# Kernel optimization log

Hardware: AMD Instinct MI355X
Metric: run time of the kernel (lower is better)

Reference implementation:

```python
import jax, jax.numpy as jnp
import numpy as np


def log_g(x):
    # log of g(x) where g(x) = x + 0.5 for x >= 0 else sigmoid(x)
    return jnp.where(x >= 0, jnp.log(jnp.where(x >= 0, x, 0.0) + 0.5), -jax.nn.softplus(-x))


def mingru_layer(x, h0, W, b):
    # x: (B,S,Din), h0: (B,1,H) positive, W: (2H,Din), b: (2H,)
    gh = jnp.einsum('bsd,ed->bse', x, W) + b
    gate, hidden = jnp.split(gh, 2, axis=-1)
    log_z = -jax.nn.softplus(-gate)        # log sigmoid(gate)
    log_coeffs = -jax.nn.softplus(gate)    # log (1 - sigmoid(gate))
    log_values = jnp.concatenate([jnp.log(h0), log_z + log_g(hidden)], axis=1)  # (B,S+1,H)
    a_star = jnp.pad(jnp.cumsum(log_coeffs, axis=1), ((0, 0), (1, 0), (0, 0)))  # (B,S+1,H)
    log_h = a_star + jax.lax.cumlogsumexp(log_values - a_star, axis=1)
    return jnp.exp(log_h)[:, 1:]  # (B,S,H)


def setup_inputs() -> dict:
    key = jax.random.key(0)
    ks = jax.random.split(key, 6)
    B, S, D, H = 8, 2048, 1024, 1024
    L = 2
    s = 0.02
    return {
        'x': jax.random.normal(ks[0], (B, S, D), jnp.float32),
        'h': jax.random.uniform(ks[1], (L, B, 1, H), jnp.float32, 0.05, 1.0),
        'w0': jax.random.normal(ks[2], (2 * H, D), jnp.float32) * s,
        'b0': jax.random.normal(ks[3], (2 * H,), jnp.float32) * s,
        'w1': jax.random.normal(ks[4], (2 * H, H), jnp.float32) * s,
        'b1': jax.random.normal(ks[5], (2 * H,), jnp.float32) * s,
    }


def reference(x, h, w0, b0, w1, b1):
    # layer 0 (residual, align = Identity since input_dims == hidden_dims)
    out0 = mingru_layer(x, h[0], w0, b0)
    h0_final = out0[:, -1:]
    inp = out0 + x
    # layer 1 (last layer: residual, no dropout after)
    out1 = mingru_layer(inp, h[1], w1, b1)
    h1_final = out1[:, -1:]
    out = out1 + inp
    h_final = jnp.stack([h0_final, h1_final])  # (L,B,1,H)
    return out, h_final
```

## Files before the change

kernel.cpp:

```cpp
#include <hip/hip_runtime.h>
#include <hip/hip_bf16.h>
#include <cstdint>
#include <cstddef>

#define GAS __attribute__((address_space(1)))
#define LAS __attribute__((address_space(3)))

typedef __attribute__((ext_vector_type(8))) __bf16 bf16x8;
typedef __attribute__((ext_vector_type(4))) float f32x4;

constexpr int kB = 8, kS = 2048, kK = 1024, kH = 1024;
constexpr int kM = kB * kS;
constexpr int kN2 = 2 * kH;
constexpr int kChunks = 64;
constexpr int kSc = kS / kChunks;

constexpr int BM = 256, BN = 256, BK = 32;
constexpr int NKT = kK / BK;

constexpr size_t kOffXb   = 0;
constexpr size_t kOffW0   = 33554432;
constexpr size_t kOffW1   = 37748736;
constexpr size_t kOffA    = 41943040;
constexpr size_t kOffG    = 75497472;
constexpr size_t kOffCA   = 109051904;
constexpr size_t kOffCV   = 111149056;
constexpr size_t kOffHst  = 113246208;
constexpr size_t kWsNeed  = 115343360;

__device__ __forceinline__ ushort f2bf(float f) {
    union { float f; uint32_t u; } v; v.f = f;
    uint32_t r = v.u + 0x7FFFu + ((v.u >> 16) & 1u);
    return (ushort)(r >> 16);
}
__device__ __forceinline__ float bf2f(ushort u) {
    union { uint32_t u; float f; } v; v.u = (uint32_t)u << 16;
    return v.f;
}

__global__ void cvt_bf16_kernel(const float* __restrict__ src, ushort* __restrict__ dst, int n4) {
    int i = blockIdx.x * blockDim.x + threadIdx.x;
    if (i >= n4) return;
    f32x4 v = *reinterpret_cast<const f32x4*>(src + (size_t)i * 4);
    ushort4 o;
    o.x = f2bf(v.x); o.y = f2bf(v.y); o.z = f2bf(v.z); o.w = f2bf(v.w);
    *reinterpret_cast<ushort4*>(dst + (size_t)i * 4) = o;
}

__global__ __launch_bounds__(512, 1)
void gemm_epi_kernel(const ushort* __restrict__ A, const ushort* __restrict__ W,
                     const float* __restrict__ bias,
                     ushort* __restrict__ abuf, ushort* __restrict__ gbuf)
{
    __shared__ ushort smem[65536];

    const int tid  = threadIdx.x;
    const int lane = tid & 63;
    const int wv   = tid >> 6;
    const int wm   = wv >> 2;
    const int wn   = wv & 3;

    const int bid = blockIdx.x;
    const int sid = (bid & 7) * 64 + (bid >> 3);
    const int tm  = sid >> 3;
    const int tn  = sid & 7;
    const int m0  = tm * BM;
    const int n0  = tn * BN;

    f32x4 acc[8][4];
#pragma unroll
    for (int i = 0; i < 8; ++i)
#pragma unroll
        for (int j = 0; j < 4; ++j) acc[i][j] = (f32x4){0.f, 0.f, 0.f, 0.f};

    const int srow  = wv * 16 + (lane >> 2);
    const int sslot = (lane & 3) ^ ((lane >> 3) & 3);
    const int scol  = sslot * 8;

    const ushort* ga0 = A + (size_t)(m0 + srow) * kK + scol;
    const ushort* ga1 = ga0 + (size_t)128 * kK;
    const ushort* gb0 = W + (size_t)(n0 + srow) * kK + scol;
    const ushort* gb1 = gb0 + (size_t)128 * kK;

    char* lds = (char*)smem;
    const int ldsw = wv * 1024;

    const int rslot = (lane >> 4) ^ ((lane >> 1) & 3);
    const int rb    = (lane & 15) * 64 + rslot * 16;
    const int aoff  = wm * 8192 + rb;
    const int boff  = 16384 + wn * 4096 + rb;

#define VMWAIT(N) asm volatile("s_waitcnt vmcnt(" #N ")" ::: "memory")

#define STAGE_A(SBUF) do {                                                       \
    __builtin_amdgcn_global_load_lds((const GAS void*)(ga0),                     \
        (LAS void*)(lds + (SBUF) * 32768 + ldsw),          16, 0, 0);            \
    __builtin_amdgcn_global_load_lds((const GAS void*)(ga1),                     \
        (LAS void*)(lds + (SBUF) * 32768 + 8192  + ldsw),  16, 0, 0);            \
  } while (0)

#define STAGE_B(SBUF) do {                                                       \
    __builtin_amdgcn_global_load_lds((const GAS void*)(gb0),                     \
        (LAS void*)(lds + (SBUF) * 32768 + 16384 + ldsw),  16, 0, 0);            \
    __builtin_amdgcn_global_load_lds((const GAS void*)(gb1),                     \
        (LAS void*)(lds + (SBUF) * 32768 + 24576 + ldsw),  16, 0, 0);            \
    ga0 += BK; ga1 += BK; gb0 += BK; gb1 += BK;                                  \
  } while (0)

#define TILE_GEN(BUF, SA, SB, EW) do {                                           \
    bf16x8 bf_[4], af_[4];                                                       \
    _Pragma("unroll")                                                            \
    for (int nf_ = 0; nf_ < 4; ++nf_)                                            \
        bf_[nf_] = *reinterpret_cast<const bf16x8*>(                             \
            lds + (BUF) * 32768 + boff + nf_ * 1024);                            \
    _Pragma("unroll")                                                            \
    for (int mf_ = 0; mf_ < 4; ++mf_)                                            \
        af_[mf_] = *reinterpret_cast<const bf16x8*>(                             \
            lds + (BUF) * 32768 + aoff + mf_ * 1024);                            \
    SA;                                                                          \
    __builtin_amdgcn_s_barrier();                                                \
    asm volatile("s_waitcnt lgkmcnt(0)" ::: "memory");                           \
    __builtin_amdgcn_sched_barrier(0);                                           \
    __builtin_amdgcn_s_setprio(1);                                               \
    _Pragma("unroll")                                                            \
    for (int mf_ = 0; mf_ < 4; ++mf_)                                            \
        _Pragma("unroll")                                                        \
        for (int nf_ = 0; nf_ < 4; ++nf_)                                        \
            acc[mf_][nf_] = __builtin_amdgcn_mfma_f32_16x16x32_bf16(             \
                af_[mf_], bf_[nf_], acc[mf_][nf_], 0, 0, 0);                     \
    __builtin_amdgcn_s_setprio(0);                                               \
    __builtin_amdgcn_s_barrier();                                                \
    _Pragma("unroll")                                                            \
    for (int mf_ = 0; mf_ < 4; ++mf_)                                            \
        af_[mf_] = *reinterpret_cast<const bf16x8*>(                             \
            lds + (BUF) * 32768 + aoff + 4096 + mf_ * 1024);                     \
    SB;                                                                          \
    __builtin_amdgcn_s_barrier();                                                \
    asm volatile("s_waitcnt lgkmcnt(0)" ::: "memory");                           \
    __builtin_amdgcn_sched_barrier(0);                                           \
    __builtin_amdgcn_s_setprio(1);                                               \
    _Pragma("unroll")                                                            \
    for (int mf_ = 0; mf_ < 4; ++mf_)                                            \
        _Pragma("unroll")                                                        \
        for (int nf_ = 0; nf_ < 4; ++nf_)                                        \
            acc[4 + mf_][nf_] = __builtin_amdgcn_mfma_f32_16x16x32_bf16(         \
                af_[mf_], bf_[nf_], acc[4 + mf_][nf_], 0, 0, 0);                 \
    __builtin_amdgcn_s_setprio(0);                                               \
    EW;                                                                          \
    __builtin_amdgcn_s_barrier();                                                \
  } while (0)

#define TILE(BUF, SBUF) TILE_GEN(BUF, STAGE_A(SBUF), STAGE_B(SBUF), VMWAIT(4))
#define TAIL0(BUF)      TILE_GEN(BUF, (void)0, (void)0, VMWAIT(0))
#define TAIL1(BUF)      TILE_GEN(BUF, (void)0, (void)0, (void)0)

    STAGE_A(0); STAGE_B(0);
    STAGE_A(1); STAGE_B(1);
    VMWAIT(4);
    __builtin_amdgcn_s_barrier();

    for (int g = 0; g < 7; ++g) {
        TILE(0, 2);
        TILE(1, 3);
        TILE(2, 0);
        TILE(3, 1);
    }
    TILE(0, 2);
    TILE(1, 3);
    TAIL0(2);
    TAIL1(3);

#undef TILE
#undef TAIL0
#undef TAIL1
#undef TILE_GEN
#undef STAGE_A
#undef STAGE_B
#undef VMWAIT

    const bool isGate = (tn < 4);
    ushort* outp = isGate ? abuf : gbuf;
    const int ncol0 = (isGate ? tn : tn - 4) * 256 + wn * 64;
    float bn[4];
#pragma unroll
    for (int nf = 0; nf < 4; ++nf) bn[nf] = bias[n0 + wn * 64 + nf * 16 + (lane & 15)];
#pragma unroll
    for (int mf = 0; mf < 8; ++mf) {
#pragma unroll
        for (int i = 0; i < 4; ++i) {
            const int m = m0 + wm * 128 + mf * 16 + (lane >> 4) * 4 + i;
            ushort* rowp = outp + (size_t)m * kH + ncol0;
#pragma unroll
            for (int nf = 0; nf < 4; ++nf) {
                float val = acc[mf][nf][i] + bn[nf];
                float r;
                if (isGate) r = 1.f / (1.f + __expf(val));
                else        r = (val >= 0.f) ? val + 0.5f : 1.f / (1.f + __expf(-val));
                rowp[nf * 16 + (lane & 15)] = f2bf(r);
            }
        }
    }
}

__global__ void scan_reduce_kernel(const ushort* __restrict__ abuf, const ushort* __restrict__ gbuf,
                                   float* __restrict__ cA, float* __restrict__ cV)
{
    int idx = blockIdx.x * 256 + threadIdx.x;
    int chg = idx & 255;
    int c   = (idx >> 8) & (kChunks - 1);
    int b   = idx >> 14;
    size_t ch = (size_t)chg * 4;
    size_t row = (size_t)b * kS + (size_t)c * kSc;
    const ushort* ap = abuf + row * kH + ch;
    const ushort* gp = gbuf + row * kH + ch;
    f32x4 A = (f32x4){1.f, 1.f, 1.f, 1.f};
    f32x4 V = (f32x4){0.f, 0.f, 0.f, 0.f};
    for (int t = 0; t < kSc; ++t) {
        ushort4 au = *reinterpret_cast<const ushort4*>(ap);
        ushort4 gu = *reinterpret_cast<const ushort4*>(gp);
        f32x4 a = (f32x4){bf2f(au.x), bf2f(au.y), bf2f(au.z), bf2f(au.w)};
        f32x4 g = (f32x4){bf2f(gu.x), bf2f(gu.y), bf2f(gu.z), bf2f(gu.w)};
        V = a * V + (1.f - a) * g;
        A = A * a;
        ap += kH; gp += kH;
    }
    size_t o = ((size_t)(b * kChunks + c) * kH) + ch;
    *reinterpret_cast<f32x4*>(cA + o) = A;
    *reinterpret_cast<f32x4*>(cV + o) = V;
}

__global__ void scan_chunks_kernel(const float* __restrict__ cA, const float* __restrict__ cV,
                                   const float* __restrict__ h0, float* __restrict__ hstart,
                                   float* __restrict__ hfin)
{
    int idx = blockIdx.x * 256 + threadIdx.x;
    int chg = idx & 255;
    int b   = idx >> 8;
    size_t ch = (size_t)chg * 4;
    f32x4 h = *reinterpret_cast<const f32x4*>(h0 + (size_t)b * kH + ch);
    for (int c = 0; c < kChunks; ++c) {
        size_t o = ((size_t)(b * kChunks + c) * kH) + ch;
        *reinterpret_cast<f32x4*>(hstart + o) = h;
        f32x4 A = *reinterpret_cast<const f32x4*>(cA + o);
        f32x4 V = *reinterpret_cast<const f32x4*>(cV + o);
        h = A * h + V;
    }
    *reinterpret_cast<f32x4*>(hfin + (size_t)b * kH + ch) = h;
}

template<bool WRITE_F32>
__global__ void scan_apply_kernel(const ushort* __restrict__ abuf, const ushort* __restrict__ gbuf,
                                  const float* __restrict__ hstart, const ushort* __restrict__ addin,
                                  void* __restrict__ outp)
{
    int idx = blockIdx.x * 256 + threadIdx.x;
    int chg = idx & 255;
    int c   = (idx >> 8) & (kChunks - 1);
    int b   = idx >> 14;
    size_t ch = (size_t)chg * 4;
    size_t row = (size_t)b * kS + (size_t)c * kSc;
    size_t base = row * kH + ch;
    f32x4 h = *reinterpret_cast<const f32x4*>(hstart + ((size_t)(b * kChunks + c) * kH) + ch);
    const ushort* ap = abuf + base;
    const ushort* gp = gbuf + base;
    for (int t = 0; t < kSc; ++t) {
        ushort4 au = *reinterpret_cast<const ushort4*>(ap);
        ushort4 gu = *reinterpret_cast<const ushort4*>(gp);
        f32x4 a = (f32x4){bf2f(au.x), bf2f(au.y), bf2f(au.z), bf2f(au.w)};
        f32x4 g = (f32x4){bf2f(gu.x), bf2f(gu.y), bf2f(gu.z), bf2f(gu.w)};
        h = a * h + (1.f - a) * g;
        ushort4 xu = *reinterpret_cast<const ushort4*>(addin + base + (size_t)t * kH);
        f32x4 r = (f32x4){bf2f(xu.x), bf2f(xu.y), bf2f(xu.z), bf2f(xu.w)};
        f32x4 o = h + r;
        if (WRITE_F32) {
            *reinterpret_cast<f32x4*>((float*)outp + base + (size_t)t * kH) = o;
        } else {
            ushort4 ob;
            ob.x = f2bf(o.x); ob.y = f2bf(o.y); ob.z = f2bf(o.z); ob.w = f2bf(o.w);
            *reinterpret_cast<ushort4*>((ushort*)outp + base + (size_t)t * kH) = ob;
        }
        ap += kH; gp += kH;
    }
}

extern "C" void kernel_launch(void* const* d_in, const int* in_sizes, int n_in,
                              void* d_out, int out_size, void* d_ws, size_t ws_size,
                              hipStream_t stream)
{
    const float* x  = (const float*)d_in[0];
    const float* h  = (const float*)d_in[1];
    const float* w0 = (const float*)d_in[2];
    const float* b0 = (const float*)d_in[3];
    const float* w1 = (const float*)d_in[4];
    const float* b1 = (const float*)d_in[5];
    float* out = (float*)d_out;
    char* ws = (char*)d_ws;

    if (ws_size < kWsNeed) return;

    ushort* xb   = (ushort*)(ws + kOffXb);
    ushort* inpb = (ushort*)(ws + kOffXb);
    ushort* w0b  = (ushort*)(ws + kOffW0);
    ushort* w1b  = (ushort*)(ws + kOffW1);
    ushort* abuf = (ushort*)(ws + kOffA);
    ushort* gbuf = (ushort*)(ws + kOffG);
    float*  cA   = (float*)(ws + kOffCA);
    float*  cV   = (float*)(ws + kOffCV);
    float*  hst  = (float*)(ws + kOffHst);

    float* out_h = out + (size_t)kM * kH;

    cvt_bf16_kernel<<<(kM * kK / 4 + 255) / 256, 256, 0, stream>>>(x, xb, kM * kK / 4);
    cvt_bf16_kernel<<<(kN2 * kK / 4 + 255) / 256, 256, 0, stream>>>(w0, w0b, kN2 * kK / 4);
    cvt_bf16_kernel<<<(kN2 * kK / 4 + 255) / 256, 256, 0, stream>>>(w1, w1b, kN2 * kK / 4);

    const int gemm_grid = (kM / BM) * (kN2 / BN);

    gemm_epi_kernel<<<gemm_grid, 512, 0, stream>>>(xb, w0b, b0, abuf, gbuf);
    scan_reduce_kernel<<<512, 256, 0, stream>>>(abuf, gbuf, cA, cV);
    scan_chunks_kernel<<<8, 256, 0, stream>>>(cA, cV, h, hst, out_h);
    scan_apply_kernel<false><<<512, 256, 0, stream>>>(abuf, gbuf, hst, xb, inpb);

    gemm_epi_kernel<<<gemm_grid, 512, 0, stream>>>(inpb, w1b, b1, abuf, gbuf);
    scan_reduce_kernel<<<512, 256, 0, stream>>>(abuf, gbuf, cA, cV);
    scan_chunks_kernel<<<8, 256, 0, stream>>>(cA, cV, h + (size_t)kB * kH, hst, out_h + (size_t)kB * kH);
    scan_apply_kernel<true><<<512, 256, 0, stream>>>(abuf, gbuf, hst, inpb, out);
}
```

Before: 289.4 us.

## Fuse chunked scan into GEMM epilogue and emit per-chunk prefix coefficients

Each GEMM tile now covers 128 gate and the matching 128 hidden columns, so the tile can stage its activations in LDS and run a local within-tile scan. It writes prefix products A and prefix values V in bf16 plus per-tile chunk summaries. This removes the separate scan_reduce pass, which had to re-read both gate buffers. A short chunk-carry kernel and a fully parallel elementwise apply kernel (h = A*hstart + V + residual) replace the serial apply loop. The cost is more LDS use, a serial scan tail inside the GEMM, and extra bf16 rounding on the prefix products.

```diff
diff --git a/kernel.cpp b/kernel.cpp
--- a/kernel.cpp
+++ b/kernel.cpp
@@ -12,9 +12,6 @@
 constexpr int kB = 8, kS = 2048, kK = 1024, kH = 1024;
 constexpr int kM = kB * kS;
 constexpr int kN2 = 2 * kH;
-constexpr int kChunks = 64;
-constexpr int kSc = kS / kChunks;
-
 constexpr int BM = 256, BN = 256, BK = 32;
 constexpr int NKT = kK / BK;
 
@@ -48,11 +45,12 @@
 }
 
 __global__ __launch_bounds__(512, 1)
-void gemm_epi_kernel(const ushort* __restrict__ A, const ushort* __restrict__ W,
-                     const float* __restrict__ bias,
-                     ushort* __restrict__ abuf, ushort* __restrict__ gbuf)
+void gemm_scan_kernel(const ushort* __restrict__ A, const ushort* __restrict__ W,
+                      const float* __restrict__ bias,
+                      ushort* __restrict__ Apref, ushort* __restrict__ Vpref,
+                      float* __restrict__ cA, float* __restrict__ cV)
 {
-    __shared__ ushort smem[65536];
+    __shared__ ushort smem[69632];
 
     const int tid  = threadIdx.x;
     const int lane = tid & 63;
@@ -65,7 +63,7 @@
     const int tm  = sid >> 3;
     const int tn  = sid & 7;
     const int m0  = tm * BM;
-    const int n0  = tn * BN;
+    const int j0  = tn * 128;
 
     f32x4 acc[8][4];
 #pragma unroll
@@ -79,8 +77,8 @@
 
     const ushort* ga0 = A + (size_t)(m0 + srow) * kK + scol;
     const ushort* ga1 = ga0 + (size_t)128 * kK;
-    const ushort* gb0 = W + (size_t)(n0 + srow) * kK + scol;
-    const ushort* gb1 = gb0 + (size_t)128 * kK;
+    const ushort* gb0 = W + (size_t)(j0 + srow) * kK + scol;
+    const ushort* gb1 = W + (size_t)(1024 + j0 + srow) * kK + scol;
 
     char* lds = (char*)smem;
     const int ldsw = wv * 1024;
@@ -178,55 +176,77 @@
 #undef STAGE_B
 #undef VMWAIT
 
-    const bool isGate = (tn < 4);
-    ushort* outp = isGate ? abuf : gbuf;
-    const int ncol0 = (isGate ? tn : tn - 4) * 256 + wn * 64;
-    float bn[4];
-#pragma unroll
-    for (int nf = 0; nf < 4; ++nf) bn[nf] = bias[n0 + wn * 64 + nf * 16 + (lane & 15)];
-#pragma unroll
-    for (int mf = 0; mf < 8; ++mf) {
-#pragma unroll
-        for (int i = 0; i < 4; ++i) {
-            const int m = m0 + wm * 128 + mf * 16 + (lane >> 4) * 4 + i;
-            ushort* rowp = outp + (size_t)m * kH + ncol0;
-#pragma unroll
-            for (int nf = 0; nf < 4; ++nf) {
-                float val = acc[mf][nf][i] + bn[nf];
-                float r;
-                if (isGate) r = 1.f / (1.f + __expf(val));
-                else        r = (val >= 0.f) ? val + 0.5f : 1.f / (1.f + __expf(-val));
-                rowp[nf * 16 + (lane & 15)] = f2bf(r);
+    ushort* a_lds = smem;
+    ushort* g_lds = smem + 33792;
+    float*  sumA  = (float*)(smem + 67584);
+    float*  sumV  = sumA + 512;
+
+    {
+        const bool isG = (wn < 2);
+        ushort* tgt = isG ? a_lds : g_lds;
+        const int jl = (wn & 1) * 64;
+        float bn[4];
+#pragma unroll
+        for (int nf = 0; nf < 4; ++nf)
+            bn[nf] = bias[(isG ? 0 : 1024) + j0 + jl + nf * 16 + (lane & 15)];
+#pragma unroll
+        for (int mf = 0; mf < 8; ++mf) {
+#pragma unroll
+            for (int i = 0; i < 4; ++i) {
+                const int m = wm * 128 + mf * 16 + (lane >> 4) * 4 + i;
+#pragma unroll
+                for (int nf = 0; nf < 4; ++nf) {
+                    float val = acc[mf][nf][i] + bn[nf];
+                    float r;
+                    if (isG) r = 1.f / (1.f + __expf(val));
+                    else     r = (val >= 0.f) ? val + 0.5f : 1.f / (1.f + __expf(-val));
+                    tgt[m * 132 + jl + nf * 16 + (lane & 15)] = f2bf(r);
+                }
             }
         }
     }
-}
-
-__global__ void scan_reduce_kernel(const ushort* __restrict__ abuf, const ushort* __restrict__ gbuf,
-                                   float* __restrict__ cA, float* __restrict__ cV)
-{
-    int idx = blockIdx.x * 256 + threadIdx.x;
-    int chg = idx & 255;
-    int c   = (idx >> 8) & (kChunks - 1);
-    int b   = idx >> 14;
-    size_t ch = (size_t)chg * 4;
-    size_t row = (size_t)b * kS + (size_t)c * kSc;
-    const ushort* ap = abuf + row * kH + ch;
-    const ushort* gp = gbuf + row * kH + ch;
-    f32x4 A = (f32x4){1.f, 1.f, 1.f, 1.f};
-    f32x4 V = (f32x4){0.f, 0.f, 0.f, 0.f};
-    for (int t = 0; t < kSc; ++t) {
-        ushort4 au = *reinterpret_cast<const ushort4*>(ap);
-        ushort4 gu = *reinterpret_cast<const ushort4*>(gp);
-        f32x4 a = (f32x4){bf2f(au.x), bf2f(au.y), bf2f(au.z), bf2f(au.w)};
-        f32x4 g = (f32x4){bf2f(gu.x), bf2f(gu.y), bf2f(gu.z), bf2f(gu.w)};
-        V = a * V + (1.f - a) * g;
-        A = A * a;
-        ap += kH; gp += kH;
-    }
-    size_t o = ((size_t)(b * kChunks + c) * kH) + ch;
-    *reinterpret_cast<f32x4*>(cA + o) = A;
-    *reinterpret_cast<f32x4*>(cV + o) = V;
+    __syncthreads();
+
+    {
+        const int j  = tid & 127;
+        const int sg = tid >> 7;
+        float A1 = 1.f, V1 = 0.f;
+#pragma unroll 4
+        for (int t = 0; t < 64; ++t) {
+            const int s = sg * 64 + t;
+            float a = bf2f(a_lds[s * 132 + j]);
+            float g = bf2f(g_lds[s * 132 + j]);
+            V1 = a * V1 + (1.f - a) * g;
+            A1 *= a;
+        }
+        sumA[sg * 128 + j] = A1;
+        sumV[sg * 128 + j] = V1;
+        __syncthreads();
+        float Ar = 1.f, Vr = 0.f;
+        for (int k = 0; k < sg; ++k) {
+            float Ak = sumA[k * 128 + j], Vk = sumV[k * 128 + j];
+            Vr = Ak * Vr + Vk;
+            Ar *= Ak;
+        }
+        ushort* ApG = Apref + (size_t)(m0 + sg * 64) * kH + j0 + j;
+        ushort* VpG = Vpref + (size_t)(m0 + sg * 64) * kH + j0 + j;
+#pragma unroll 4
+        for (int t = 0; t < 64; ++t) {
+            const int s = sg * 64 + t;
+            float a = bf2f(a_lds[s * 132 + j]);
+            float g = bf2f(g_lds[s * 132 + j]);
+            Vr = a * Vr + (1.f - a) * g;
+            Ar *= a;
+            *ApG = f2bf(Ar);
+            *VpG = f2bf(Vr);
+            ApG += kH; VpG += kH;
+        }
+        if (sg == 3) {
+            const int b = tm >> 3, c = tm & 7;
+            cA[((b * 8 + c) << 10) + j0 + j] = Ar;
+            cV[((b * 8 + c) << 10) + j0 + j] = Vr;
+        }
+    }
 }
 
 __global__ void scan_chunks_kernel(const float* __restrict__ cA, const float* __restrict__ cV,
@@ -234,52 +254,40 @@
                                    float* __restrict__ hfin)
 {
     int idx = blockIdx.x * 256 + threadIdx.x;
-    int chg = idx & 255;
-    int b   = idx >> 8;
-    size_t ch = (size_t)chg * 4;
-    f32x4 h = *reinterpret_cast<const f32x4*>(h0 + (size_t)b * kH + ch);
-    for (int c = 0; c < kChunks; ++c) {
-        size_t o = ((size_t)(b * kChunks + c) * kH) + ch;
-        *reinterpret_cast<f32x4*>(hstart + o) = h;
-        f32x4 A = *reinterpret_cast<const f32x4*>(cA + o);
-        f32x4 V = *reinterpret_cast<const f32x4*>(cV + o);
-        h = A * h + V;
-    }
-    *reinterpret_cast<f32x4*>(hfin + (size_t)b * kH + ch) = h;
+    int j = idx & 1023, b = idx >> 10;
+    float h = h0[(b << 10) + j];
+    for (int c = 0; c < 8; ++c) {
+        int o = ((b * 8 + c) << 10) + j;
+        hstart[o] = h;
+        h = cA[o] * h + cV[o];
+    }
+    hfin[(b << 10) + j] = h;
 }
 
 template<bool WRITE_F32>
-__global__ void scan_apply_kernel(const ushort* __restrict__ abuf, const ushort* __restrict__ gbuf,
-                                  const float* __restrict__ hstart, const ushort* __restrict__ addin,
-                                  void* __restrict__ outp)
+__global__ void apply_kernel(const ushort* __restrict__ Ap, const ushort* __restrict__ Vp,
+                             const float* __restrict__ hst, const ushort* __restrict__ res,
+                             void* __restrict__ outp)
 {
-    int idx = blockIdx.x * 256 + threadIdx.x;
-    int chg = idx & 255;
-    int c   = (idx >> 8) & (kChunks - 1);
-    int b   = idx >> 14;
-    size_t ch = (size_t)chg * 4;
-    size_t row = (size_t)b * kS + (size_t)c * kSc;
-    size_t base = row * kH + ch;
-    f32x4 h = *reinterpret_cast<const f32x4*>(hstart + ((size_t)(b * kChunks + c) * kH) + ch);
-    const ushort* ap = abuf + base;
-    const ushort* gp = gbuf + base;
-    for (int t = 0; t < kSc; ++t) {
-        ushort4 au = *reinterpret_cast<const ushort4*>(ap);
-        ushort4 gu = *reinterpret_cast<const ushort4*>(gp);
-        f32x4 a = (f32x4){bf2f(au.x), bf2f(au.y), bf2f(au.z), bf2f(au.w)};
-        f32x4 g = (f32x4){bf2f(gu.x), bf2f(gu.y), bf2f(gu.z), bf2f(gu.w)};
-        h = a * h + (1.f - a) * g;
-        ushort4 xu = *reinterpret_cast<const ushort4*>(addin + base + (size_t)t * kH);
-        f32x4 r = (f32x4){bf2f(xu.x), bf2f(xu.y), bf2f(xu.z), bf2f(xu.w)};
-        f32x4 o = h + r;
-        if (WRITE_F32) {
-            *reinterpret_cast<f32x4*>((float*)outp + base + (size_t)t * kH) = o;
-        } else {
-            ushort4 ob;
-            ob.x = f2bf(o.x); ob.y = f2bf(o.y); ob.z = f2bf(o.z); ob.w = f2bf(o.w);
-            *reinterpret_cast<ushort4*>((ushort*)outp + base + (size_t)t * kH) = ob;
-        }
-        ap += kH; gp += kH;
+    size_t i = ((size_t)blockIdx.x * 256 + threadIdx.x) * 4;
+    int m = (int)(i >> 10);
+    int j = (int)(i & 1023);
+    int b = m >> 11, s = m & 2047, c = s >> 8;
+    f32x4 hcs = *reinterpret_cast<const f32x4*>(hst + (((b * 8 + c) << 10) + j));
+    ushort4 Au = *reinterpret_cast<const ushort4*>(Ap + i);
+    ushort4 Vu = *reinterpret_cast<const ushort4*>(Vp + i);
+    ushort4 Ru = *reinterpret_cast<const ushort4*>(res + i);
+    f32x4 o;
+    o.x = bf2f(Au.x) * hcs.x + bf2f(Vu.x) + bf2f(Ru.x);
+    o.y = bf2f(Au.y) * hcs.y + bf2f(Vu.y) + bf2f(Ru.y);
+    o.z = bf2f(Au.z) * hcs.z + bf2f(Vu.z) + bf2f(Ru.z);
+    o.w = bf2f(Au.w) * hcs.w + bf2f(Vu.w) + bf2f(Ru.w);
+    if (WRITE_F32) {
+        *reinterpret_cast<f32x4*>((float*)outp + i) = o;
+    } else {
+        ushort4 ob;
+        ob.x = f2bf(o.x); ob.y = f2bf(o.y); ob.z = f2bf(o.z); ob.w = f2bf(o.w);
+        *reinterpret_cast<ushort4*>((ushort*)outp + i) = ob;
     }
 }
 
@@ -302,8 +310,8 @@
     ushort* inpb = (ushort*)(ws + kOffXb);
     ushort* w0b  = (ushort*)(ws + kOffW0);
     ushort* w1b  = (ushort*)(ws + kOffW1);
-    ushort* abuf = (ushort*)(ws + kOffA);
-    ushort* gbuf = (ushort*)(ws + kOffG);
+    ushort* Ap   = (ushort*)(ws + kOffA);
+    ushort* Vp   = (ushort*)(ws + kOffG);
     float*  cA   = (float*)(ws + kOffCA);
     float*  cV   = (float*)(ws + kOffCV);
     float*  hst  = (float*)(ws + kOffHst);
@@ -314,15 +322,14 @@
     cvt_bf16_kernel<<<(kN2 * kK / 4 + 255) / 256, 256, 0, stream>>>(w0, w0b, kN2 * kK / 4);
     cvt_bf16_kernel<<<(kN2 * kK / 4 + 255) / 256, 256, 0, stream>>>(w1, w1b, kN2 * kK / 4);
 
-    const int gemm_grid = (kM / BM) * (kN2 / BN);
-
-    gemm_epi_kernel<<<gemm_grid, 512, 0, stream>>>(xb, w0b, b0, abuf, gbuf);
-    scan_reduce_kernel<<<512, 256, 0, stream>>>(abuf, gbuf, cA, cV);
-    scan_chunks_kernel<<<8, 256, 0, stream>>>(cA, cV, h, hst, out_h);
-    scan_apply_kernel<false><<<512, 256, 0, stream>>>(abuf, gbuf, hst, xb, inpb);
-
-    gemm_epi_kernel<<<gemm_grid, 512, 0, stream>>>(inpb, w1b, b1, abuf, gbuf);
-    scan_reduce_kernel<<<512, 256, 0, stream>>>(abuf, gbuf, cA, cV);
-    scan_chunks_kernel<<<8, 256, 0, stream>>>(cA, cV, h + (size_t)kB * kH, hst, out_h + (size_t)kB * kH);
-    scan_apply_kernel<true><<<512, 256, 0, stream>>>(abuf, gbuf, hst, inpb, out);
-}
+    const int gemm_grid  = (kM / BM) * (kN2 / BN);
+    const int apply_grid = kM * kH / 4 / 256;
+
+    gemm_scan_kernel<<<gemm_grid, 512, 0, stream>>>(xb, w0b, b0, Ap, Vp, cA, cV);
+    scan_chunks_kernel<<<32, 256, 0, stream>>>(cA, cV, h, hst, out_h);
+    apply_kernel<false><<<apply_grid, 256, 0, stream>>>(Ap, Vp, hst, xb, inpb);
+
+    gemm_scan_kernel<<<gemm_grid, 512, 0, stream>>>(inpb, w1b, b1, Ap, Vp, cA, cV);
+    scan_chunks_kernel<<<32, 256, 0, stream>>>(cA, cV, h + (size_t)kB * kH, hst, out_h + (size_t)kB * kH);
+    apply_kernel<true><<<apply_grid, 256, 0, stream>>>(Ap, Vp, hst, inpb, out);
+}
```

Measured after the change: 272.1 us. 1.06x faster.
